# Kernel optimization log

Measured on AMD Instinct MI355X. Metric: run time of the kernel, lower is better.

The kernel has to match this reference:

```python
import jax, jax.numpy as jnp
import numpy as np
from jax import lax

NUM_HEADS = 8
LN_EPS = 1e-5


def setup_inputs() -> dict:
    key = jax.random.key(0)
    ks = jax.random.split(key, 24)
    B, N, ENC = 64, 49, 2048
    V, E, A, D, T1 = 32000, 512, 512, 512, 21
    s = 0.02
    inp = {
        "encoder_outputs": jax.random.normal(ks[0], (B, N, ENC), jnp.float32),
        "captions": jax.random.randint(ks[1], (B, T1), 0, V),
        # embedding ~ U(-0.1, 0.1) per _init_weights
        "embedding_w": jax.random.uniform(ks[2], (V, E), jnp.float32, -0.1, 0.1),
        # multi-head attention params (attention_dim = A, heads = NUM_HEADS)
        "Wq": jax.random.normal(ks[3], (D, A), jnp.float32) * s,
        "bq": jnp.zeros((A,), jnp.float32),
        "Wk": jax.random.normal(ks[4], (ENC, A), jnp.float32) * s,
        "bk": jnp.zeros((A,), jnp.float32),
        "Wv": jax.random.normal(ks[5], (ENC, A), jnp.float32) * s,
        "bv": jnp.zeros((A,), jnp.float32),
        "Wo": jax.random.normal(ks[6], (A, ENC), jnp.float32) * s,
        "bo": jnp.zeros((ENC,), jnp.float32),
        # init_h: Linear(encoder_dim, decoder_dim), torch layout [out, in]
        "init_w": jax.random.normal(ks[7], (D, ENC), jnp.float32) * s,
        "init_b": jnp.zeros((D,), jnp.float32),
        # GRUCell(input = E + ENC, hidden = D), torch layout
        "W_ih": jax.random.normal(ks[8], (3 * D, E + ENC), jnp.float32) * s,
        "b_ih": jnp.zeros((3 * D,), jnp.float32),
        "W_hh": jax.random.normal(ks[9], (3 * D, D), jnp.float32) * s,
        "b_hh": jnp.zeros((3 * D,), jnp.float32),
        "ln_g": jnp.ones((D,), jnp.float32),
        "ln_b": jnp.zeros((D,), jnp.float32),
        # fc ~ U(-0.1, 0.1), bias 0 per _init_weights
        "fc_w": jax.random.uniform(ks[10], (V, D), jnp.float32, -0.1, 0.1),
        "fc_b": jnp.zeros((V,), jnp.float32),
    }
    return inp


def reference(encoder_outputs, captions, embedding_w, Wq, bq, Wk, bk, Wv, bv,
              Wo, bo, init_w, init_b, W_ih, b_ih, W_hh, b_hh, ln_g, ln_b,
              fc_w, fc_b):
    B, N, ENC = encoder_outputs.shape
    T = captions.shape[1] - 1
    A = Wq.shape[1]
    hd = A // NUM_HEADS
    scale = 1.0 / np.sqrt(hd)

    # embeddings for teacher-forcing inputs: [B, T, E]
    emb = embedding_w[captions[:, :T]]
    # initial hidden: Linear(mean over features)
    h0 = encoder_outputs.mean(axis=1) @ init_w.T + init_b  # [B, D]
    # K/V depend only on encoder features -> compute once
    k = (encoder_outputs @ Wk + bk).reshape(B, N, NUM_HEADS, hd)
    v = (encoder_outputs @ Wv + bv).reshape(B, N, NUM_HEADS, hd)

    def step(h, emb_t):
        q = (h @ Wq + bq).reshape(B, NUM_HEADS, hd)
        scores = jnp.einsum('bhd,bnhd->bhn', q, k) * scale
        alpha = jax.nn.softmax(scores, axis=-1)            # [B, H, N]
        ctx = jnp.einsum('bhn,bnhd->bhd', alpha, v).reshape(B, A)
        attn_out = ctx @ Wo + bo                           # [B, ENC]
        x = jnp.concatenate([emb_t, attn_out], axis=1)     # [B, E+ENC]
        gi = x @ W_ih.T + b_ih
        gh = h @ W_hh.T + b_hh
        ir, iz, inn = jnp.split(gi, 3, axis=1)
        hr, hz, hn = jnp.split(gh, 3, axis=1)
        r = jax.nn.sigmoid(ir + hr)
        z = jax.nn.sigmoid(iz + hz)
        n = jnp.tanh(inn + r * hn)
        h_new = (1.0 - z) * n + z * h
        # layernorm
        mu = h_new.mean(axis=-1, keepdims=True)
        var = jnp.mean(jnp.square(h_new - mu), axis=-1, keepdims=True)
        h_ln = (h_new - mu) * lax.rsqrt(var + LN_EPS) * ln_g + ln_b
        # dropout in eval mode -> identity
        logits = h_ln @ fc_w.T + fc_b                      # [B, V]
        return h_ln, (logits, alpha.mean(axis=1))

    _, (outs, attns) = lax.scan(step, h0, jnp.swapaxes(emb, 0, 1))
    outputs = jnp.swapaxes(outs, 0, 1)            # [B, T, V]
    attention_weights = jnp.swapaxes(attns, 0, 1) # [B, T, N]
    return outputs, attention_weights
```

## Files before the change

kernel.cpp:

```cpp
#include <hip/hip_runtime.h>
#include <hip/hip_bf16.h>
#include <math.h>


#define TSTEPS 20

#define OFF_ME      0u
#define OFF_EMBALL  131072u
#define OFF_KT      786432u
#define OFF_V       2392064u
#define OFF_GIE     3997696u
#define OFF_WF      5963776u
#define OFF_GIBO    6750208u
#define OFF_H       6751744u
#define OFF_HALL    6784512u
#define OFF_H0P     7439872u
#define OFF_QP      7702016u
#define OFF_GHP     7833088u
#define OFF_GIP     8226304u
#define OFF_CTX     8619520u

__global__ void mean_kernel(const float* __restrict__ enc, float* __restrict__ me) {
    int i = blockIdx.x * 256 + threadIdx.x;
    int b = i >> 11, e = i & 2047;
    const float* p = enc + (size_t)b * 49 * 2048 + e;
    float s = 0.f;
    #pragma unroll 7
    for (int n = 0; n < 49; n++) s += p[n * 2048];
    me[i] = s * (1.0f / 49.0f);
}

__global__ void init_kernel(const int* __restrict__ captions, const float* __restrict__ emb_w,
                            float* __restrict__ embAll, float* __restrict__ attw) {
    int i = blockIdx.x * 256 + threadIdx.x;
    int t = i >> 15;
    int b = (i >> 9) & 63;
    int e = i & 511;
    int tok = captions[b * 21 + t];
    embAll[i] = emb_w[(size_t)tok * 512 + e];
    if (i < 62720) attw[i] = 0.f;
}

__global__ void gibo_kernel(const float* __restrict__ W_ih, const float* __restrict__ bo,
                            float* __restrict__ gibo) {
    int j = blockIdx.x, tid = threadIdx.x;
    const float* w = W_ih + (size_t)j * 2560 + 512;
    float s = 0.f;
    for (int e = tid; e < 2048; e += 256) s += w[e] * bo[e];
    for (int o = 32; o; o >>= 1) s += __shfl_xor(s, o);
    __shared__ float r[4];
    if ((tid & 63) == 0) r[tid >> 6] = s;
    __syncthreads();
    if (tid == 0) gibo[j] = r[0] + r[1] + r[2] + r[3];
}

__global__ __launch_bounds__(256) void gemm_splitk(
    const float* __restrict__ A, int lda,
    const float* __restrict__ Bm, int ldb, int bt,
    float* __restrict__ Cp, int N, int KC) {
    __shared__ float As[16][68];
    __shared__ float Bs[16][68];
    int tid = threadIdx.x;
    int n0 = blockIdx.x * 64;
    int k0base = blockIdx.y * KC;
    int tn = tid & 15, tm = tid >> 4;
    float acc[4][4] = {};
    int am = tid >> 2, akq = (tid & 3) * 4;
    for (int kk = 0; kk < KC; kk += 16) {
        int k0 = k0base + kk;
        float4 av = *(const float4*)(A + (size_t)am * lda + k0 + akq);
        if (bt == 0) {
            int bk = tid >> 4, bn = (tid & 15) * 4;
            float4 bv = *(const float4*)(Bm + (size_t)(k0 + bk) * ldb + n0 + bn);
            *(float4*)&Bs[bk][bn] = bv;
        } else {
            int bn = tid >> 2, bkq = (tid & 3) * 4;
            float4 bv = *(const float4*)(Bm + (size_t)(n0 + bn) * ldb + k0 + bkq);
            Bs[bkq + 0][bn] = bv.x; Bs[bkq + 1][bn] = bv.y;
            Bs[bkq + 2][bn] = bv.z; Bs[bkq + 3][bn] = bv.w;
        }
        As[akq + 0][am] = av.x; As[akq + 1][am] = av.y;
        As[akq + 2][am] = av.z; As[akq + 3][am] = av.w;
        __syncthreads();
        #pragma unroll
        for (int k = 0; k < 16; k++) {
            float4 a4 = *(const float4*)&As[k][tm * 4];
            float4 b4 = *(const float4*)&Bs[k][tn * 4];
            float a_[4] = {a4.x, a4.y, a4.z, a4.w};
            float b_[4] = {b4.x, b4.y, b4.z, b4.w};
            #pragma unroll
            for (int i = 0; i < 4; i++)
                #pragma unroll
                for (int j = 0; j < 4; j++) acc[i][j] += a_[i] * b_[j];
        }
        __syncthreads();
    }
    float* cp = Cp + (size_t)blockIdx.y * 64 * N + n0;
    #pragma unroll
    for (int i = 0; i < 4; i++) {
        float4 o = make_float4(acc[i][0], acc[i][1], acc[i][2], acc[i][3]);
        *(float4*)(cp + (size_t)(tm * 4 + i) * N + tn * 4) = o;
    }
}

__global__ __launch_bounds__(256) void gemm128(
    const float* __restrict__ A, int lda, int M,
    const float* __restrict__ Bm, int ldb, int bt,
    const float* __restrict__ bias,
    float* __restrict__ C, int ldc, int K, int emode) {
    __shared__ float As[16][136];
    __shared__ float Bs[16][136];
    int tid = threadIdx.x;
    int n0 = blockIdx.x * 128, m0 = blockIdx.y * 128;
    int tn = tid & 15, tm = tid >> 4;
    float acc[8][8] = {};
    for (int k0 = 0; k0 < K; k0 += 16) {
        {
            int m = tid >> 1, kq = (tid & 1) * 8;
            int gm = m0 + m;
            float4 v0 = make_float4(0, 0, 0, 0), v1 = make_float4(0, 0, 0, 0);
            if (gm < M) {
                v0 = *(const float4*)(A + (size_t)gm * lda + k0 + kq);
                v1 = *(const float4*)(A + (size_t)gm * lda + k0 + kq + 4);
            }
            As[kq + 0][m] = v0.x; As[kq + 1][m] = v0.y; As[kq + 2][m] = v0.z; As[kq + 3][m] = v0.w;
            As[kq + 4][m] = v1.x; As[kq + 5][m] = v1.y; As[kq + 6][m] = v1.z; As[kq + 7][m] = v1.w;
        }
        if (bt) {
            int n = tid >> 1, kq = (tid & 1) * 8;
            float4 v0 = *(const float4*)(Bm + (size_t)(n0 + n) * ldb + k0 + kq);
            float4 v1 = *(const float4*)(Bm + (size_t)(n0 + n) * ldb + k0 + kq + 4);
            Bs[kq + 0][n] = v0.x; Bs[kq + 1][n] = v0.y; Bs[kq + 2][n] = v0.z; Bs[kq + 3][n] = v0.w;
            Bs[kq + 4][n] = v1.x; Bs[kq + 5][n] = v1.y; Bs[kq + 6][n] = v1.z; Bs[kq + 7][n] = v1.w;
        } else {
            int bk = tid >> 4, n8 = (tid & 15) * 8;
            float4 v0 = *(const float4*)(Bm + (size_t)(k0 + bk) * ldb + n0 + n8);
            float4 v1 = *(const float4*)(Bm + (size_t)(k0 + bk) * ldb + n0 + n8 + 4);
            *(float4*)&Bs[bk][n8] = v0;
            *(float4*)&Bs[bk][n8 + 4] = v1;
        }
        __syncthreads();
        #pragma unroll
        for (int k = 0; k < 16; k++) {
            float4 a0 = *(const float4*)&As[k][tm * 8];
            float4 a1 = *(const float4*)&As[k][tm * 8 + 4];
            float4 b0 = *(const float4*)&Bs[k][tn * 4];
            float4 b1 = *(const float4*)&Bs[k][64 + tn * 4];
            float a_[8] = {a0.x, a0.y, a0.z, a0.w, a1.x, a1.y, a1.z, a1.w};
            float b_[8] = {b0.x, b0.y, b0.z, b0.w, b1.x, b1.y, b1.z, b1.w};
            #pragma unroll
            for (int i = 0; i < 8; i++)
                #pragma unroll
                for (int j = 0; j < 8; j++) acc[i][j] += a_[i] * b_[j];
        }
        __syncthreads();
    }
    float bvals[8];
    #pragma unroll
    for (int j = 0; j < 8; j++) {
        int col = (j < 4) ? (n0 + tn * 4 + j) : (n0 + 64 + tn * 4 + j - 4);
        bvals[j] = bias ? bias[col] : 0.f;
    }
    #pragma unroll
    for (int i = 0; i < 8; i++) {
        int gm = m0 + tm * 8 + i;
        if (gm >= M) break;
        if (emode == 0) {
            float* cp = C + (size_t)gm * ldc;
            float4 o0 = make_float4(acc[i][0] + bvals[0], acc[i][1] + bvals[1],
                                    acc[i][2] + bvals[2], acc[i][3] + bvals[3]);
            float4 o1 = make_float4(acc[i][4] + bvals[4], acc[i][5] + bvals[5],
                                    acc[i][6] + bvals[6], acc[i][7] + bvals[7]);
            *(float4*)(cp + n0 + tn * 4) = o0;
            *(float4*)(cp + n0 + 64 + tn * 4) = o1;
        } else if (emode == 1) {
            int orow = (gm & 63) * TSTEPS + (gm >> 6);
            float* cp = C + (size_t)orow * ldc;
            float4 o0 = make_float4(acc[i][0] + bvals[0], acc[i][1] + bvals[1],
                                    acc[i][2] + bvals[2], acc[i][3] + bvals[3]);
            float4 o1 = make_float4(acc[i][4] + bvals[4], acc[i][5] + bvals[5],
                                    acc[i][6] + bvals[6], acc[i][7] + bvals[7]);
            *(float4*)(cp + n0 + tn * 4) = o0;
            *(float4*)(cp + n0 + 64 + tn * 4) = o1;
        } else {
            int bb = gm / 49, nn2 = gm - bb * 49;
            #pragma unroll
            for (int j = 0; j < 8; j++) {
                int col = (j < 4) ? (n0 + tn * 4 + j) : (n0 + 64 + tn * 4 + j - 4);
                int hh = col >> 6, dd = col & 63;
                C[((size_t)(bb * 8 + hh) * 64 + dd) * 49 + nn2] = acc[i][j] + bvals[j];
            }
        }
    }
}

__global__ void reduce_h0(const float* __restrict__ h0p, const float* __restrict__ init_b,
                          float* __restrict__ h) {
    int i = blockIdx.x * 256 + threadIdx.x;
    float s = init_b[i & 511];
    #pragma unroll
    for (int z = 0; z < 8; z++) s += h0p[z * 32768 + i];
    h[i] = s;
}

__global__ void attn_kernel(const float* __restrict__ qp, const float* __restrict__ bq,
                            const float* __restrict__ kt, const float* __restrict__ v,
                            float* __restrict__ ctx, float* __restrict__ attw, int t) {
    int bh = blockIdx.x;
    int b = bh >> 3, hh = bh & 7;
    int lane = threadIdx.x;
    __shared__ float qs[64];
    __shared__ float al[49];
    float qv = bq[hh * 64 + lane];
    #pragma unroll
    for (int s = 0; s < 4; s++) qv += qp[s * 32768 + b * 512 + hh * 64 + lane];
    qs[lane] = qv;
    __syncthreads();
    float sc = -1e30f;
    if (lane < 49) {
        const float* kp = kt + (size_t)bh * 64 * 49 + lane;
        float a = 0.f;
        #pragma unroll 8
        for (int d = 0; d < 64; d++) a += qs[d] * kp[d * 49];
        sc = a * 0.125f;
    }
    float mx = sc;
    for (int o = 32; o; o >>= 1) mx = fmaxf(mx, __shfl_xor(mx, o));
    float e = (lane < 49) ? expf(sc - mx) : 0.f;
    float sm = e;
    for (int o = 32; o; o >>= 1) sm += __shfl_xor(sm, o);
    float a = e / sm;
    if (lane < 49) {
        al[lane] = a;
        atomicAdd(&attw[(size_t)(b * TSTEPS + t) * 49 + lane], a * 0.125f);
    }
    __syncthreads();
    const float* vp = v + (size_t)b * 49 * 512 + hh * 64 + lane;
    float c = 0.f;
    #pragma unroll 7
    for (int n = 0; n < 49; n++) c += al[n] * vp[n * 512];
    ctx[b * 512 + hh * 64 + lane] = c;
}

__global__ void gate_ln_kernel(const float* __restrict__ gip, const float* __restrict__ ghp,
                               const float* __restrict__ giE, const float* __restrict__ gibo,
                               const float* __restrict__ b_ih, const float* __restrict__ b_hh,
                               const float* __restrict__ ln_g, const float* __restrict__ ln_b,
                               float* __restrict__ h, float* __restrict__ h_all, int t) {
    int b = blockIdx.x, d = threadIdx.x;
    const float* gie = giE + (size_t)(t * 64 + b) * 1536;
    float g0 = b_ih[d] + gibo[d] + gie[d];
    float g1 = b_ih[512 + d] + gibo[512 + d] + gie[512 + d];
    float g2 = b_ih[1024 + d] + gibo[1024 + d] + gie[1024 + d];
    float e0 = b_hh[d], e1 = b_hh[512 + d], e2 = b_hh[1024 + d];
    #pragma unroll
    for (int s = 0; s < 4; s++) {
        const float* gp = gip + (size_t)s * 98304 + b * 1536;
        const float* hp = ghp + (size_t)s * 98304 + b * 1536;
        g0 += gp[d]; g1 += gp[512 + d]; g2 += gp[1024 + d];
        e0 += hp[d]; e1 += hp[512 + d]; e2 += hp[1024 + d];
    }
    float r = 1.f / (1.f + expf(-(g0 + e0)));
    float z = 1.f / (1.f + expf(-(g1 + e1)));
    float nn = tanhf(g2 + r * e2);
    float hprev = h[b * 512 + d];
    float hn = (1.f - z) * nn + z * hprev;
    __shared__ float red[8];
    float x = hn;
    for (int o = 32; o; o >>= 1) x += __shfl_xor(x, o);
    if ((d & 63) == 0) red[d >> 6] = x;
    __syncthreads();
    float mu = 0.f;
    #pragma unroll
    for (int i = 0; i < 8; i++) mu += red[i];
    mu *= (1.f / 512.f);
    __syncthreads();
    float c = hn - mu;
    x = c * c;
    for (int o = 32; o; o >>= 1) x += __shfl_xor(x, o);
    if ((d & 63) == 0) red[d >> 6] = x;
    __syncthreads();
    float var = 0.f;
    #pragma unroll
    for (int i = 0; i < 8; i++) var += red[i];
    var *= (1.f / 512.f);
    float hl = c * rsqrtf(var + 1e-5f) * ln_g[d] + ln_b[d];
    h[b * 512 + d] = hl;
    h_all[(size_t)(t * 64 + b) * 512 + d] = hl;
}

extern "C" void kernel_launch(void* const* d_in, const int* in_sizes, int n_in,
                              void* d_out, int out_size, void* d_ws, size_t ws_size,
                              hipStream_t stream) {
    const float* enc     = (const float*)d_in[0];
    const int*   caps    = (const int*)d_in[1];
    const float* emb_w   = (const float*)d_in[2];
    const float* Wq      = (const float*)d_in[3];
    const float* bq      = (const float*)d_in[4];
    const float* Wk      = (const float*)d_in[5];
    const float* bk      = (const float*)d_in[6];
    const float* Wv      = (const float*)d_in[7];
    const float* bv      = (const float*)d_in[8];
    const float* Wo      = (const float*)d_in[9];
    const float* bo      = (const float*)d_in[10];
    const float* init_w  = (const float*)d_in[11];
    const float* init_b  = (const float*)d_in[12];
    const float* W_ih    = (const float*)d_in[13];
    const float* b_ih    = (const float*)d_in[14];
    const float* W_hh    = (const float*)d_in[15];
    const float* b_hh    = (const float*)d_in[16];
    const float* ln_g    = (const float*)d_in[17];
    const float* ln_b    = (const float*)d_in[18];
    const float* fc_w    = (const float*)d_in[19];
    const float* fc_b    = (const float*)d_in[20];

    float* ws     = (float*)d_ws;
    float* me     = ws + OFF_ME;
    float* embAll = ws + OFF_EMBALL;
    float* ktb    = ws + OFF_KT;
    float* vb     = ws + OFF_V;
    float* giE    = ws + OFF_GIE;
    float* Wfused = ws + OFF_WF;
    float* gibo   = ws + OFF_GIBO;
    float* h      = ws + OFF_H;
    float* h_all  = ws + OFF_HALL;
    float* h0p    = ws + OFF_H0P;
    float* qp     = ws + OFF_QP;
    float* ghp    = ws + OFF_GHP;
    float* gip    = ws + OFF_GIP;
    float* ctx    = ws + OFF_CTX;

    float* out    = (float*)d_out;
    float* attw   = out + 40960000;

    hipLaunchKernelGGL(mean_kernel, dim3(512), dim3(256), 0, stream, enc, me);
    hipLaunchKernelGGL(init_kernel, dim3(2560), dim3(256), 0, stream, caps, emb_w, embAll, attw);
    hipLaunchKernelGGL(gibo_kernel, dim3(1536), dim3(256), 0, stream, W_ih, bo, gibo);
    hipLaunchKernelGGL(gemm_splitk, dim3(8, 8), dim3(256), 0, stream,
                       me, 2048, init_w, 2048, 1, h0p, 512, 256);
    hipLaunchKernelGGL(reduce_h0, dim3(128), dim3(256), 0, stream, h0p, init_b, h);
    hipLaunchKernelGGL(gemm128, dim3(4, 25), dim3(256), 0, stream,
                       enc, 2048, 3136, Wk, 512, 0, bk, ktb, 0, 2048, 2);
    hipLaunchKernelGGL(gemm128, dim3(4, 25), dim3(256), 0, stream,
                       enc, 2048, 3136, Wv, 512, 0, bv, vb, 512, 2048, 0);
    hipLaunchKernelGGL(gemm128, dim3(12, 10), dim3(256), 0, stream,
                       embAll, 512, 1280, W_ih, 2560, 1, (const float*)nullptr, giE, 1536, 512, 0);
    hipLaunchKernelGGL(gemm128, dim3(12, 4), dim3(256), 0, stream,
                       Wo, 2048, 512, W_ih + 512, 2560, 1, (const float*)nullptr, Wfused, 1536, 2048, 0);

    for (int t = 0; t < TSTEPS; t++) {
        hipLaunchKernelGGL(gemm_splitk, dim3(8, 4), dim3(256), 0, stream,
                           h, 512, Wq, 512, 0, qp, 512, 128);
        hipLaunchKernelGGL(gemm_splitk, dim3(24, 4), dim3(256), 0, stream,
                           h, 512, W_hh, 512, 1, ghp, 1536, 128);
        hipLaunchKernelGGL(attn_kernel, dim3(512), dim3(64), 0, stream,
                           qp, bq, ktb, vb, ctx, attw, t);
        hipLaunchKernelGGL(gemm_splitk, dim3(24, 4), dim3(256), 0, stream,
                           ctx, 512, Wfused, 1536, 0, gip, 1536, 128);
        hipLaunchKernelGGL(gate_ln_kernel, dim3(64), dim3(512), 0, stream,
                           gip, ghp, giE, gibo, b_ih, b_hh, ln_g, ln_b, h, h_all, t);
    }

    hipLaunchKernelGGL(gemm128, dim3(250, 10), dim3(256), 0, stream,
                       h_all, 512, 1280, fc_w, 512, 1, fc_b, out, 32000, 512, 1);
}
```

Before: 2.593 ms.

## Use bf16 MFMA for logits, fuse per-step kernels, replace GEMM tiles

The final vocabulary projection now runs on bf16 MFMA instructions. The hidden states are split into high and low bf16 parts so the activation side keeps near-fp32 precision, while the fc weights are converted once to bf16. The per-step Wq/W_hh/attention kernels are fused into one step kernel, and split-K partial buffers with their reductions are removed. All fp32 GEMMs move to a new 1024-thread 64x64 tile kernel. Rounding fc weights to bf16 loses precision, and the new fp32 tile has low per-thread work, which may hurt efficiency in the setup GEMMs.

Result: slower. 4.194 ms (+61.7%).

```diff
diff --git a/kernel.cpp b/kernel.cpp
--- a/kernel.cpp
+++ b/kernel.cpp
@@ -1,24 +1,44 @@
 #include <hip/hip_runtime.h>
-#include <hip/hip_bf16.h>
 #include <math.h>
 
 
 #define TSTEPS 20
+#define AS_LD 65
+#define BS_LD 68
 
 #define OFF_ME      0u
-#define OFF_EMBALL  131072u
+#define OFF_EMB     131072u
 #define OFF_KT      786432u
 #define OFF_V       2392064u
 #define OFF_GIE     3997696u
 #define OFF_WF      5963776u
 #define OFF_GIBO    6750208u
 #define OFF_H       6751744u
-#define OFF_HALL    6784512u
-#define OFF_H0P     7439872u
-#define OFF_QP      7702016u
-#define OFF_GHP     7833088u
-#define OFF_GIP     8226304u
-#define OFF_CTX     8619520u
+#define OFF_GHP     6784512u
+#define OFF_GIP     6882816u
+#define OFF_CTX     6981120u
+#define OFF_HALLH   7013888u
+#define OFF_HALLL   7341568u
+#define OFF_FCH     7669248u
+
+typedef __bf16 bf16x8 __attribute__((ext_vector_type(8)));
+typedef float f32x4 __attribute__((ext_vector_type(4)));
+
+__device__ __forceinline__ unsigned short f2bf(float x) {
+    unsigned u = __float_as_uint(x);
+    unsigned r = (u + 0x7fffu + ((u >> 16) & 1u)) >> 16;
+    return (unsigned short)r;
+}
+__device__ __forceinline__ float bf2f(unsigned short h) {
+    return __uint_as_float(((unsigned)h) << 16);
+}
+
+__device__ __forceinline__ void gload16(const void* g, void* l) {
+    __builtin_amdgcn_global_load_lds(
+        (const __attribute__((address_space(1))) unsigned int*)g,
+        (__attribute__((address_space(3))) unsigned int*)l, 16, 0, 0);
+}
+
 
 __global__ void mean_kernel(const float* __restrict__ enc, float* __restrict__ me) {
     int i = blockIdx.x * 256 + threadIdx.x;
@@ -54,212 +74,179 @@
     if (tid == 0) gibo[j] = r[0] + r[1] + r[2] + r[3];
 }
 
-__global__ __launch_bounds__(256) void gemm_splitk(
+__global__ void conv_fc(const float* __restrict__ fc, unsigned short* __restrict__ outp) {
+    int i = (blockIdx.x * 256 + threadIdx.x) * 4;
+    float4 v = *(const float4*)(fc + i);
+    unsigned h0 = f2bf(v.x), h1 = f2bf(v.y), h2 = f2bf(v.z), h3 = f2bf(v.w);
+    uint2 o;
+    o.x = h0 | (h1 << 16);
+    o.y = h2 | (h3 << 16);
+    *(uint2*)(outp + i) = o;
+}
+
+
+__device__ __forceinline__ void gemm_tile_1024(
+    const float* __restrict__ A, int lda, int m0,
+    const float* __restrict__ B, int ldb, int bt, int n0, int K,
+    float* As, float* Bs, float acc[4]) {
+    int tid = threadIdx.x;
+    int r = tid & 63, c0 = (tid >> 6) * 4;
+    acc[0] = acc[1] = acc[2] = acc[3] = 0.f;
+    for (int k0 = 0; k0 < K; k0 += 64) {
+        {
+            int m = tid >> 4, kq = (tid & 15) * 4;
+            float4 av = *(const float4*)(A + (size_t)(m0 + m) * lda + k0 + kq);
+            As[(kq + 0) * AS_LD + m] = av.x;
+            As[(kq + 1) * AS_LD + m] = av.y;
+            As[(kq + 2) * AS_LD + m] = av.z;
+            As[(kq + 3) * AS_LD + m] = av.w;
+        }
+        if (bt == 0) {
+            int k = tid >> 4, nq = (tid & 15) * 4;
+            *(float4*)&Bs[k * BS_LD + nq] =
+                *(const float4*)(B + (size_t)(k0 + k) * ldb + n0 + nq);
+        } else {
+            int n = tid >> 4, kq = (tid & 15) * 4;
+            float4 bv = *(const float4*)(B + (size_t)(n0 + n) * ldb + k0 + kq);
+            Bs[(kq + 0) * BS_LD + n] = bv.x;
+            Bs[(kq + 1) * BS_LD + n] = bv.y;
+            Bs[(kq + 2) * BS_LD + n] = bv.z;
+            Bs[(kq + 3) * BS_LD + n] = bv.w;
+        }
+        __syncthreads();
+        #pragma unroll 8
+        for (int k = 0; k < 64; k++) {
+            float a = As[k * AS_LD + r];
+            float4 b4 = *(const float4*)&Bs[k * BS_LD + c0];
+            acc[0] += a * b4.x;
+            acc[1] += a * b4.y;
+            acc[2] += a * b4.z;
+            acc[3] += a * b4.w;
+        }
+        __syncthreads();
+    }
+}
+
+__global__ __launch_bounds__(1024) void gemm64f(
     const float* __restrict__ A, int lda,
-    const float* __restrict__ Bm, int ldb, int bt,
-    float* __restrict__ Cp, int N, int KC) {
-    __shared__ float As[16][68];
-    __shared__ float Bs[16][68];
-    int tid = threadIdx.x;
-    int n0 = blockIdx.x * 64;
-    int k0base = blockIdx.y * KC;
-    int tn = tid & 15, tm = tid >> 4;
-    float acc[4][4] = {};
-    int am = tid >> 2, akq = (tid & 3) * 4;
-    for (int kk = 0; kk < KC; kk += 16) {
-        int k0 = k0base + kk;
-        float4 av = *(const float4*)(A + (size_t)am * lda + k0 + akq);
-        if (bt == 0) {
-            int bk = tid >> 4, bn = (tid & 15) * 4;
-            float4 bv = *(const float4*)(Bm + (size_t)(k0 + bk) * ldb + n0 + bn);
-            *(float4*)&Bs[bk][bn] = bv;
-        } else {
-            int bn = tid >> 2, bkq = (tid & 3) * 4;
-            float4 bv = *(const float4*)(Bm + (size_t)(n0 + bn) * ldb + k0 + bkq);
-            Bs[bkq + 0][bn] = bv.x; Bs[bkq + 1][bn] = bv.y;
-            Bs[bkq + 2][bn] = bv.z; Bs[bkq + 3][bn] = bv.w;
-        }
-        As[akq + 0][am] = av.x; As[akq + 1][am] = av.y;
-        As[akq + 2][am] = av.z; As[akq + 3][am] = av.w;
-        __syncthreads();
-        #pragma unroll
-        for (int k = 0; k < 16; k++) {
-            float4 a4 = *(const float4*)&As[k][tm * 4];
-            float4 b4 = *(const float4*)&Bs[k][tn * 4];
-            float a_[4] = {a4.x, a4.y, a4.z, a4.w};
-            float b_[4] = {b4.x, b4.y, b4.z, b4.w};
-            #pragma unroll
-            for (int i = 0; i < 4; i++)
-                #pragma unroll
-                for (int j = 0; j < 4; j++) acc[i][j] += a_[i] * b_[j];
-        }
-        __syncthreads();
-    }
-    float* cp = Cp + (size_t)blockIdx.y * 64 * N + n0;
-    #pragma unroll
-    for (int i = 0; i < 4; i++) {
-        float4 o = make_float4(acc[i][0], acc[i][1], acc[i][2], acc[i][3]);
-        *(float4*)(cp + (size_t)(tm * 4 + i) * N + tn * 4) = o;
-    }
-}
-
-__global__ __launch_bounds__(256) void gemm128(
-    const float* __restrict__ A, int lda, int M,
-    const float* __restrict__ Bm, int ldb, int bt,
+    const float* __restrict__ B, int ldb, int bt,
     const float* __restrict__ bias,
     float* __restrict__ C, int ldc, int K, int emode) {
-    __shared__ float As[16][136];
-    __shared__ float Bs[16][136];
+    __shared__ float As[64 * AS_LD];
+    __shared__ float Bs[64 * BS_LD];
+    int m0 = blockIdx.y * 64, n0 = blockIdx.x * 64;
+    float acc[4];
+    gemm_tile_1024(A, lda, m0, B, ldb, bt, n0, K, As, Bs, acc);
     int tid = threadIdx.x;
-    int n0 = blockIdx.x * 128, m0 = blockIdx.y * 128;
-    int tn = tid & 15, tm = tid >> 4;
-    float acc[8][8] = {};
-    for (int k0 = 0; k0 < K; k0 += 16) {
-        {
-            int m = tid >> 1, kq = (tid & 1) * 8;
-            int gm = m0 + m;
-            float4 v0 = make_float4(0, 0, 0, 0), v1 = make_float4(0, 0, 0, 0);
-            if (gm < M) {
-                v0 = *(const float4*)(A + (size_t)gm * lda + k0 + kq);
-                v1 = *(const float4*)(A + (size_t)gm * lda + k0 + kq + 4);
-            }
-            As[kq + 0][m] = v0.x; As[kq + 1][m] = v0.y; As[kq + 2][m] = v0.z; As[kq + 3][m] = v0.w;
-            As[kq + 4][m] = v1.x; As[kq + 5][m] = v1.y; As[kq + 6][m] = v1.z; As[kq + 7][m] = v1.w;
-        }
-        if (bt) {
-            int n = tid >> 1, kq = (tid & 1) * 8;
-            float4 v0 = *(const float4*)(Bm + (size_t)(n0 + n) * ldb + k0 + kq);
-            float4 v1 = *(const float4*)(Bm + (size_t)(n0 + n) * ldb + k0 + kq + 4);
-            Bs[kq + 0][n] = v0.x; Bs[kq + 1][n] = v0.y; Bs[kq + 2][n] = v0.z; Bs[kq + 3][n] = v0.w;
-            Bs[kq + 4][n] = v1.x; Bs[kq + 5][n] = v1.y; Bs[kq + 6][n] = v1.z; Bs[kq + 7][n] = v1.w;
-        } else {
-            int bk = tid >> 4, n8 = (tid & 15) * 8;
-            float4 v0 = *(const float4*)(Bm + (size_t)(k0 + bk) * ldb + n0 + n8);
-            float4 v1 = *(const float4*)(Bm + (size_t)(k0 + bk) * ldb + n0 + n8 + 4);
-            *(float4*)&Bs[bk][n8] = v0;
-            *(float4*)&Bs[bk][n8 + 4] = v1;
-        }
-        __syncthreads();
-        #pragma unroll
-        for (int k = 0; k < 16; k++) {
-            float4 a0 = *(const float4*)&As[k][tm * 8];
-            float4 a1 = *(const float4*)&As[k][tm * 8 + 4];
-            float4 b0 = *(const float4*)&Bs[k][tn * 4];
-            float4 b1 = *(const float4*)&Bs[k][64 + tn * 4];
-            float a_[8] = {a0.x, a0.y, a0.z, a0.w, a1.x, a1.y, a1.z, a1.w};
-            float b_[8] = {b0.x, b0.y, b0.z, b0.w, b1.x, b1.y, b1.z, b1.w};
-            #pragma unroll
-            for (int i = 0; i < 8; i++)
-                #pragma unroll
-                for (int j = 0; j < 8; j++) acc[i][j] += a_[i] * b_[j];
-        }
-        __syncthreads();
-    }
-    float bvals[8];
-    #pragma unroll
-    for (int j = 0; j < 8; j++) {
-        int col = (j < 4) ? (n0 + tn * 4 + j) : (n0 + 64 + tn * 4 + j - 4);
-        bvals[j] = bias ? bias[col] : 0.f;
-    }
-    #pragma unroll
-    for (int i = 0; i < 8; i++) {
-        int gm = m0 + tm * 8 + i;
-        if (gm >= M) break;
-        if (emode == 0) {
-            float* cp = C + (size_t)gm * ldc;
-            float4 o0 = make_float4(acc[i][0] + bvals[0], acc[i][1] + bvals[1],
-                                    acc[i][2] + bvals[2], acc[i][3] + bvals[3]);
-            float4 o1 = make_float4(acc[i][4] + bvals[4], acc[i][5] + bvals[5],
-                                    acc[i][6] + bvals[6], acc[i][7] + bvals[7]);
-            *(float4*)(cp + n0 + tn * 4) = o0;
-            *(float4*)(cp + n0 + 64 + tn * 4) = o1;
-        } else if (emode == 1) {
-            int orow = (gm & 63) * TSTEPS + (gm >> 6);
-            float* cp = C + (size_t)orow * ldc;
-            float4 o0 = make_float4(acc[i][0] + bvals[0], acc[i][1] + bvals[1],
-                                    acc[i][2] + bvals[2], acc[i][3] + bvals[3]);
-            float4 o1 = make_float4(acc[i][4] + bvals[4], acc[i][5] + bvals[5],
-                                    acc[i][6] + bvals[6], acc[i][7] + bvals[7]);
-            *(float4*)(cp + n0 + tn * 4) = o0;
-            *(float4*)(cp + n0 + 64 + tn * 4) = o1;
-        } else {
-            int bb = gm / 49, nn2 = gm - bb * 49;
-            #pragma unroll
-            for (int j = 0; j < 8; j++) {
-                int col = (j < 4) ? (n0 + tn * 4 + j) : (n0 + 64 + tn * 4 + j - 4);
-                int hh = col >> 6, dd = col & 63;
-                C[((size_t)(bb * 8 + hh) * 64 + dd) * 49 + nn2] = acc[i][j] + bvals[j];
-            }
-        }
-    }
-}
-
-__global__ void reduce_h0(const float* __restrict__ h0p, const float* __restrict__ init_b,
-                          float* __restrict__ h) {
-    int i = blockIdx.x * 256 + threadIdx.x;
-    float s = init_b[i & 511];
-    #pragma unroll
-    for (int z = 0; z < 8; z++) s += h0p[z * 32768 + i];
-    h[i] = s;
-}
-
-__global__ void attn_kernel(const float* __restrict__ qp, const float* __restrict__ bq,
-                            const float* __restrict__ kt, const float* __restrict__ v,
-                            float* __restrict__ ctx, float* __restrict__ attw, int t) {
-    int bh = blockIdx.x;
-    int b = bh >> 3, hh = bh & 7;
-    int lane = threadIdx.x;
-    __shared__ float qs[64];
-    __shared__ float al[49];
-    float qv = bq[hh * 64 + lane];
-    #pragma unroll
-    for (int s = 0; s < 4; s++) qv += qp[s * 32768 + b * 512 + hh * 64 + lane];
-    qs[lane] = qv;
-    __syncthreads();
-    float sc = -1e30f;
-    if (lane < 49) {
-        const float* kp = kt + (size_t)bh * 64 * 49 + lane;
-        float a = 0.f;
-        #pragma unroll 8
-        for (int d = 0; d < 64; d++) a += qs[d] * kp[d * 49];
-        sc = a * 0.125f;
-    }
-    float mx = sc;
-    for (int o = 32; o; o >>= 1) mx = fmaxf(mx, __shfl_xor(mx, o));
-    float e = (lane < 49) ? expf(sc - mx) : 0.f;
-    float sm = e;
-    for (int o = 32; o; o >>= 1) sm += __shfl_xor(sm, o);
-    float a = e / sm;
-    if (lane < 49) {
-        al[lane] = a;
-        atomicAdd(&attw[(size_t)(b * TSTEPS + t) * 49 + lane], a * 0.125f);
-    }
-    __syncthreads();
-    const float* vp = v + (size_t)b * 49 * 512 + hh * 64 + lane;
-    float c = 0.f;
-    #pragma unroll 7
-    for (int n = 0; n < 49; n++) c += al[n] * vp[n * 512];
-    ctx[b * 512 + hh * 64 + lane] = c;
-}
-
-__global__ void gate_ln_kernel(const float* __restrict__ gip, const float* __restrict__ ghp,
-                               const float* __restrict__ giE, const float* __restrict__ gibo,
-                               const float* __restrict__ b_ih, const float* __restrict__ b_hh,
-                               const float* __restrict__ ln_g, const float* __restrict__ ln_b,
-                               float* __restrict__ h, float* __restrict__ h_all, int t) {
+    int r = tid & 63, c0 = (tid >> 6) * 4;
+    int gm = m0 + r;
+    if (emode == 0) {
+        float4 o;
+        o.x = acc[0] + (bias ? bias[n0 + c0 + 0] : 0.f);
+        o.y = acc[1] + (bias ? bias[n0 + c0 + 1] : 0.f);
+        o.z = acc[2] + (bias ? bias[n0 + c0 + 2] : 0.f);
+        o.w = acc[3] + (bias ? bias[n0 + c0 + 3] : 0.f);
+        *(float4*)(C + (size_t)gm * ldc + n0 + c0) = o;
+    } else {
+        int bb = gm / 49, nn2 = gm - bb * 49;
+        #pragma unroll
+        for (int j = 0; j < 4; j++) {
+            int col = n0 + c0 + j;
+            int hh = col >> 6, dd = col & 63;
+            C[((size_t)(bb * 8 + hh) * 64 + dd) * 49 + nn2] = acc[j] + bias[col];
+        }
+    }
+}
+
+
+__global__ __launch_bounds__(1024) void step1_kernel(
+    const float* __restrict__ h, const float* __restrict__ Wq, const float* __restrict__ bq,
+    const float* __restrict__ Whh, const float* __restrict__ ktb, const float* __restrict__ vb,
+    float* __restrict__ ctx, float* __restrict__ ghp, float* __restrict__ attw, int t) {
+    __shared__ float As[64 * AS_LD];
+    __shared__ float Bs[64 * BS_LD];
+    __shared__ float qs[64 * 65];
+    __shared__ float al[64 * 52];
+    int blk = blockIdx.x, tid = threadIdx.x;
+    float acc[4];
+    if (blk >= 8) {
+        int n0 = (blk - 8) * 64;
+        gemm_tile_1024(h, 512, 0, Whh, 512, 1, n0, 512, As, Bs, acc);
+        int r = tid & 63, c0 = (tid >> 6) * 4;
+        float4 o = make_float4(acc[0], acc[1], acc[2], acc[3]);
+        *(float4*)(ghp + (size_t)r * 1536 + n0 + c0) = o;
+        return;
+    }
+    int hh = blk;
+    gemm_tile_1024(h, 512, 0, Wq, 512, 0, hh * 64, 512, As, Bs, acc);
+    {
+        int r = tid & 63, c0 = (tid >> 6) * 4;
+        #pragma unroll
+        for (int j = 0; j < 4; j++) qs[r * 65 + c0 + j] = acc[j] + bq[hh * 64 + c0 + j];
+    }
+    __syncthreads();
+    {
+        int b = tid >> 4, jj = tid & 15;
+        float sv[4];
+        int nn[4];
+        int cnt = 0;
+        #pragma unroll
+        for (int i = 0; i < 4; i++) {
+            int n = jj + 16 * i;
+            if (n < 49) { nn[cnt] = n; sv[cnt] = 0.f; cnt++; }
+        }
+        const float* kpb = ktb + ((size_t)(b * 8 + hh) * 64) * 49;
+        for (int d = 0; d < 64; d++) {
+            float qv = qs[b * 65 + d];
+            const float* kp = kpb + d * 49;
+            for (int c = 0; c < cnt; c++) sv[c] += qv * kp[nn[c]];
+        }
+        float mx = -1e30f;
+        for (int c = 0; c < cnt; c++) { sv[c] *= 0.125f; mx = fmaxf(mx, sv[c]); }
+        for (int o = 8; o; o >>= 1) mx = fmaxf(mx, __shfl_xor(mx, o));
+        float sm = 0.f;
+        for (int c = 0; c < cnt; c++) { sv[c] = expf(sv[c] - mx); sm += sv[c]; }
+        for (int o = 8; o; o >>= 1) sm += __shfl_xor(sm, o);
+        float inv = 1.f / sm;
+        for (int c = 0; c < cnt; c++) {
+            float a = sv[c] * inv;
+            al[b * 52 + nn[c]] = a;
+            atomicAdd(&attw[(size_t)(b * TSTEPS + t) * 49 + nn[c]], a * 0.125f);
+        }
+    }
+    __syncthreads();
+    {
+        int d = tid & 63, bg = tid >> 6;
+        #pragma unroll
+        for (int bb = 0; bb < 4; bb++) {
+            int b2 = bg * 4 + bb;
+            const float* vp = vb + (size_t)b2 * 49 * 512 + hh * 64 + d;
+            const float* alp = al + b2 * 52;
+            float c = 0.f;
+            #pragma unroll 7
+            for (int n = 0; n < 49; n++) c += alp[n] * vp[(size_t)n * 512];
+            ctx[b2 * 512 + hh * 64 + d] = c;
+        }
+    }
+}
+
+__global__ __launch_bounds__(512) void gate_ln_kernel(
+    const float* __restrict__ gip, const float* __restrict__ ghp,
+    const float* __restrict__ giE, const float* __restrict__ gibo,
+    const float* __restrict__ b_ih, const float* __restrict__ b_hh,
+    const float* __restrict__ ln_g, const float* __restrict__ ln_b,
+    float* __restrict__ h, unsigned short* __restrict__ hallH,
+    unsigned short* __restrict__ hallL, int t) {
     int b = blockIdx.x, d = threadIdx.x;
     const float* gie = giE + (size_t)(t * 64 + b) * 1536;
-    float g0 = b_ih[d] + gibo[d] + gie[d];
-    float g1 = b_ih[512 + d] + gibo[512 + d] + gie[512 + d];
-    float g2 = b_ih[1024 + d] + gibo[1024 + d] + gie[1024 + d];
-    float e0 = b_hh[d], e1 = b_hh[512 + d], e2 = b_hh[1024 + d];
-    #pragma unroll
-    for (int s = 0; s < 4; s++) {
-        const float* gp = gip + (size_t)s * 98304 + b * 1536;
-        const float* hp = ghp + (size_t)s * 98304 + b * 1536;
-        g0 += gp[d]; g1 += gp[512 + d]; g2 += gp[1024 + d];
-        e0 += hp[d]; e1 += hp[512 + d]; e2 += hp[1024 + d];
-    }
+    const float* gp = gip + (size_t)b * 1536;
+    const float* hp = ghp + (size_t)b * 1536;
+    float g0 = gp[d] + gie[d] + b_ih[d] + gibo[d];
+    float g1 = gp[512 + d] + gie[512 + d] + b_ih[512 + d] + gibo[512 + d];
+    float g2 = gp[1024 + d] + gie[1024 + d] + b_ih[1024 + d] + gibo[1024 + d];
+    float e0 = hp[d] + b_hh[d];
+    float e1 = hp[512 + d] + b_hh[512 + d];
+    float e2 = hp[1024 + d] + b_hh[1024 + d];
     float r = 1.f / (1.f + expf(-(g0 + e0)));
     float z = 1.f / (1.f + expf(-(g1 + e1)));
     float nn = tanhf(g2 + r * e2);
@@ -286,81 +273,140 @@
     var *= (1.f / 512.f);
     float hl = c * rsqrtf(var + 1e-5f) * ln_g[d] + ln_b[d];
     h[b * 512 + d] = hl;
-    h_all[(size_t)(t * 64 + b) * 512 + d] = hl;
-}
+    unsigned short hi = f2bf(hl);
+    hallH[(size_t)(t * 64 + b) * 512 + d] = hi;
+    hallL[(size_t)(t * 64 + b) * 512 + d] = f2bf(hl - bf2f(hi));
+}
+
+__global__ __launch_bounds__(256) void logits_mfma(
+    const unsigned short* __restrict__ Ahi, const unsigned short* __restrict__ Alo,
+    const unsigned short* __restrict__ Bhi, const float* __restrict__ bias,
+    float* __restrict__ out) {
+    __shared__ __align__(16) short As[128 * 64];
+    __shared__ __align__(16) short Bs[128 * 64];
+    int tid = threadIdx.x;
+    int wid = tid >> 6, lane = tid & 63;
+    int n0 = blockIdx.x * 128, m0 = blockIdx.y * 128;
+    f32x4 acc[4][4] = {};
+    int wm = (wid >> 1) * 64, wn = (wid & 1) * 64;
+    int crow = lane & 15;
+    int koff8 = (lane >> 4) * 8;
+    for (int k0e = 0; k0e < 1024; k0e += 64) {
+        const unsigned short* Ab = (k0e & 512) ? Alo : Ahi;
+        int koff = k0e & 511;
+        #pragma unroll
+        for (int c = 0; c < 4; c++) {
+            int chunk = wid * 4 + c;
+            int off = chunk * 512 + lane * 8;
+            int row = off >> 6, col = off & 63;
+            gload16(Ab + (size_t)(m0 + row) * 512 + koff + col, &As[chunk * 512]);
+            gload16(Bhi + (size_t)(n0 + row) * 512 + koff + col, &Bs[chunk * 512]);
+        }
+        __syncthreads();
+        #pragma unroll
+        for (int ks = 0; ks < 2; ks++) {
+            bf16x8 af[4], bfm[4];
+            #pragma unroll
+            for (int i = 0; i < 4; i++)
+                af[i] = *(const bf16x8*)&As[(wm + i * 16 + crow) * 64 + ks * 32 + koff8];
+            #pragma unroll
+            for (int j = 0; j < 4; j++)
+                bfm[j] = *(const bf16x8*)&Bs[(wn + j * 16 + crow) * 64 + ks * 32 + koff8];
+            #pragma unroll
+            for (int i = 0; i < 4; i++)
+                #pragma unroll
+                for (int j = 0; j < 4; j++)
+                    acc[i][j] = __builtin_amdgcn_mfma_f32_16x16x32_bf16(
+                        af[i], bfm[j], acc[i][j], 0, 0, 0);
+        }
+        __syncthreads();
+    }
+    int r4 = (lane >> 4) * 4;
+    #pragma unroll
+    for (int i = 0; i < 4; i++) {
+        #pragma unroll
+        for (int j = 0; j < 4; j++) {
+            int col = n0 + wn + j * 16 + (lane & 15);
+            float bv = bias[col];
+            #pragma unroll
+            for (int r = 0; r < 4; r++) {
+                int gm = m0 + wm + i * 16 + r4 + r;
+                int orow = (gm & 63) * TSTEPS + (gm >> 6);
+                out[(size_t)orow * 32000 + col] = acc[i][j][r] + bv;
+            }
+        }
+    }
+}
+
 
 extern "C" void kernel_launch(void* const* d_in, const int* in_sizes, int n_in,
                               void* d_out, int out_size, void* d_ws, size_t ws_size,
                               hipStream_t stream) {
-    const float* enc     = (const float*)d_in[0];
-    const int*   caps    = (const int*)d_in[1];
-    const float* emb_w   = (const float*)d_in[2];
-    const float* Wq      = (const float*)d_in[3];
-    const float* bq      = (const float*)d_in[4];
-    const float* Wk      = (const float*)d_in[5];
-    const float* bk      = (const float*)d_in[6];
-    const float* Wv      = (const float*)d_in[7];
-    const float* bv      = (const float*)d_in[8];
-    const float* Wo      = (const float*)d_in[9];
-    const float* bo      = (const float*)d_in[10];
-    const float* init_w  = (const float*)d_in[11];
-    const float* init_b  = (const float*)d_in[12];
-    const float* W_ih    = (const float*)d_in[13];
-    const float* b_ih    = (const float*)d_in[14];
-    const float* W_hh    = (const float*)d_in[15];
-    const float* b_hh    = (const float*)d_in[16];
-    const float* ln_g    = (const float*)d_in[17];
-    const float* ln_b    = (const float*)d_in[18];
-    const float* fc_w    = (const float*)d_in[19];
-    const float* fc_b    = (const float*)d_in[20];
+    const float* enc    = (const float*)d_in[0];
+    const int*   caps   = (const int*)d_in[1];
+    const float* emb_w  = (const float*)d_in[2];
+    const float* Wq     = (const float*)d_in[3];
+    const float* bq     = (const float*)d_in[4];
+    const float* Wk     = (const float*)d_in[5];
+    const float* bk     = (const float*)d_in[6];
+    const float* Wv     = (const float*)d_in[7];
+    const float* bv     = (const float*)d_in[8];
+    const float* Wo     = (const float*)d_in[9];
+    const float* bo     = (const float*)d_in[10];
+    const float* init_w = (const float*)d_in[11];
+    const float* init_b = (const float*)d_in[12];
+    const float* W_ih   = (const float*)d_in[13];
+    const float* b_ih   = (const float*)d_in[14];
+    const float* W_hh   = (const float*)d_in[15];
+    const float* b_hh   = (const float*)d_in[16];
+    const float* ln_g   = (const float*)d_in[17];
+    const float* ln_b   = (const float*)d_in[18];
+    const float* fc_w   = (const float*)d_in[19];
+    const float* fc_b   = (const float*)d_in[20];
 
     float* ws     = (float*)d_ws;
     float* me     = ws + OFF_ME;
-    float* embAll = ws + OFF_EMBALL;
+    float* embAll = ws + OFF_EMB;
     float* ktb    = ws + OFF_KT;
     float* vb     = ws + OFF_V;
     float* giE    = ws + OFF_GIE;
     float* Wfused = ws + OFF_WF;
     float* gibo   = ws + OFF_GIBO;
     float* h      = ws + OFF_H;
-    float* h_all  = ws + OFF_HALL;
-    float* h0p    = ws + OFF_H0P;
-    float* qp     = ws + OFF_QP;
     float* ghp    = ws + OFF_GHP;
     float* gip    = ws + OFF_GIP;
     float* ctx    = ws + OFF_CTX;
-
-    float* out    = (float*)d_out;
-    float* attw   = out + 40960000;
+    unsigned short* hallH = (unsigned short*)(ws + OFF_HALLH);
+    unsigned short* hallL = (unsigned short*)(ws + OFF_HALLL);
+    unsigned short* fcH   = (unsigned short*)(ws + OFF_FCH);
+
+    float* out  = (float*)d_out;
+    float* attw = out + 40960000;
 
     hipLaunchKernelGGL(mean_kernel, dim3(512), dim3(256), 0, stream, enc, me);
     hipLaunchKernelGGL(init_kernel, dim3(2560), dim3(256), 0, stream, caps, emb_w, embAll, attw);
     hipLaunchKernelGGL(gibo_kernel, dim3(1536), dim3(256), 0, stream, W_ih, bo, gibo);
-    hipLaunchKernelGGL(gemm_splitk, dim3(8, 8), dim3(256), 0, stream,
-                       me, 2048, init_w, 2048, 1, h0p, 512, 256);
-    hipLaunchKernelGGL(reduce_h0, dim3(128), dim3(256), 0, stream, h0p, init_b, h);
-    hipLaunchKernelGGL(gemm128, dim3(4, 25), dim3(256), 0, stream,
-                       enc, 2048, 3136, Wk, 512, 0, bk, ktb, 0, 2048, 2);
-    hipLaunchKernelGGL(gemm128, dim3(4, 25), dim3(256), 0, stream,
-                       enc, 2048, 3136, Wv, 512, 0, bv, vb, 512, 2048, 0);
-    hipLaunchKernelGGL(gemm128, dim3(12, 10), dim3(256), 0, stream,
-                       embAll, 512, 1280, W_ih, 2560, 1, (const float*)nullptr, giE, 1536, 512, 0);
-    hipLaunchKernelGGL(gemm128, dim3(12, 4), dim3(256), 0, stream,
-                       Wo, 2048, 512, W_ih + 512, 2560, 1, (const float*)nullptr, Wfused, 1536, 2048, 0);
+    hipLaunchKernelGGL(conv_fc, dim3(16000), dim3(256), 0, stream, fc_w, fcH);
+    hipLaunchKernelGGL(gemm64f, dim3(8, 1), dim3(1024), 0, stream,
+                       me, 2048, init_w, 2048, 1, init_b, h, 512, 2048, 0);
+    hipLaunchKernelGGL(gemm64f, dim3(8, 49), dim3(1024), 0, stream,
+                       enc, 2048, Wk, 512, 0, bk, ktb, 0, 2048, 2);
+    hipLaunchKernelGGL(gemm64f, dim3(8, 49), dim3(1024), 0, stream,
+                       enc, 2048, Wv, 512, 0, bv, vb, 512, 2048, 0);
+    hipLaunchKernelGGL(gemm64f, dim3(24, 20), dim3(1024), 0, stream,
+                       embAll, 512, W_ih, 2560, 1, (const float*)nullptr, giE, 1536, 512, 0);
+    hipLaunchKernelGGL(gemm64f, dim3(24, 8), dim3(1024), 0, stream,
+                       Wo, 2048, W_ih + 512, 2560, 1, (const float*)nullptr, Wfused, 1536, 2048, 0);
 
     for (int t = 0; t < TSTEPS; t++) {
-        hipLaunchKernelGGL(gemm_splitk, dim3(8, 4), dim3(256), 0, stream,
-                           h, 512, Wq, 512, 0, qp, 512, 128);
-        hipLaunchKernelGGL(gemm_splitk, dim3(24, 4), dim3(256), 0, stream,
-                           h, 512, W_hh, 512, 1, ghp, 1536, 128);
-        hipLaunchKernelGGL(attn_kernel, dim3(512), dim3(64), 0, stream,
-                           qp, bq, ktb, vb, ctx, attw, t);
-        hipLaunchKernelGGL(gemm_splitk, dim3(24, 4), dim3(256), 0, stream,
-                           ctx, 512, Wfused, 1536, 0, gip, 1536, 128);
+        hipLaunchKernelGGL(step1_kernel, dim3(32), dim3(1024), 0, stream,
+                           h, Wq, bq, W_hh, ktb, vb, ctx, ghp, attw, t);
+        hipLaunchKernelGGL(gemm64f, dim3(24, 1), dim3(1024), 0, stream,
+                           ctx, 512, Wfused, 1536, 0, (const float*)nullptr, gip, 1536, 512, 0);
         hipLaunchKernelGGL(gate_ln_kernel, dim3(64), dim3(512), 0, stream,
-                           gip, ghp, giE, gibo, b_ih, b_hh, ln_g, ln_b, h, h_all, t);
-    }
-
-    hipLaunchKernelGGL(gemm128, dim3(250, 10), dim3(256), 0, stream,
-                       h_all, 512, 1280, fc_w, 512, 1, fc_b, out, 32000, 512, 1);
-}
+                           gip, ghp, giE, gibo, b_ih, b_hh, ln_g, ln_b, h, hallH, hallL, t);
+    }
+
+    hipLaunchKernelGGL(logits_mfma, dim3(250, 10), dim3(256), 0, stream,
+                       hallH, hallL, fcH, fc_b, out);
+}
```
